# Optimization experiments

Hardware: AMD Instinct MI355X
Metric: run time of the kernel (lower is better)

## Reference

```python
import jax, jax.numpy as jnp
import numpy as np

N = 50000      # nodes
E = 800000     # edges (avg degree 16)
D = 128        # hidden dim
L = 3          # message-passing layers
NU = 1         # DRew nu -> delay = max(k - nu, 0)


def setup_inputs() -> dict:
    key = jax.random.key(0)
    ks = jax.random.split(key, 6)
    x = jax.random.normal(ks[0], (N, D), dtype=jnp.float32)
    edge_index = jax.random.randint(ks[1], (2, E), 0, N)          # [2, E] (src, dst)
    edge_attr = jax.random.randint(ks[2], (E,), 1, L + 1)          # edge types in {1..L}
    scale = 1.0 / np.sqrt(D).astype(np.float32)
    Ws = jax.random.normal(ks[3], (L, D, D), dtype=jnp.float32) * scale       # mlp_s per layer
    bs = jnp.zeros((L, D), dtype=jnp.float32)
    Wk = jax.random.normal(ks[4], (L, L, D, D), dtype=jnp.float32) * scale    # mlp_k, padded; layer t uses k=1..t+1
    bk = jnp.zeros((L, L, D), dtype=jnp.float32)
    eps = jnp.zeros((L,), dtype=jnp.float32)
    return dict(x=x, edge_index=edge_index, edge_attr=edge_attr,
                Ws=Ws, bs=bs, Wk=Wk, bk=bk, eps=eps)


def reference(x, edge_index, edge_attr, Ws, bs, Wk, bk, eps):
    src, dst = edge_index[0], edge_index[1]
    xs = [x]
    for t in range(L):
        xt = xs[-1]
        # out = (1 + eps) * mlp_s(x)
        out = (1.0 + eps[t]) * jax.nn.relu(xt @ Ws[t] + bs[t])
        for k in range(1, t + 2):
            delay = max(k - NU, 0)
            x_src = xs[t - delay]                       # delayed node features
            mask = (edge_attr == k).astype(xt.dtype)    # edge-type mask (replaces boolean column select)
            msg = x_src[src] * mask[:, None]            # gather + mask: [E, D]
            agg = jax.ops.segment_sum(msg, dst, num_segments=N)  # scatter-add per destination
            out = out + jax.nn.relu(agg @ Wk[t, k - 1] + bk[t, k - 1])  # mlp_k(k)
        # gin_nn_post is an empty Sequential -> identity; then F.relu; then residual
        h = jax.nn.relu(out)
        xs.append(xt + h)
    return xs[-1]
```

## Files before the change

kernel.cpp:

```cpp
#include <hip/hip_runtime.h>
#include <hip/hip_bf16.h>


#define NODES 50000
#define EDGES 800000
#define DIM   128
#define ND    ((long)NODES * DIM)
#define NB3   (3 * NODES)
#define NPART 8
#define PSIZE (NODES / NPART)
#define NROWP 50048
#define NBLKS ((NB3 + 255) / 256)
#define NCELL 192
#define SORTN (NCELL * NBLKS)

typedef __attribute__((ext_vector_type(8))) short  bf16x8;
typedef __attribute__((ext_vector_type(4))) float  f32x4;

#define LDS_STRIDE 136

__global__ __launch_bounds__(256) void init_kernel(
    const float* __restrict__ x, const float* __restrict__ Ws,
    const float* __restrict__ Wk, __hip_bfloat16* __restrict__ xb0,
    __hip_bfloat16* __restrict__ xb1, __hip_bfloat16* __restrict__ xb2,
    __hip_bfloat16* __restrict__ WT, int* __restrict__ cursor) {
  int b = blockIdx.x, tid = threadIdx.x;
  long i = (long)b * 256 + tid;
  if (i < ND / 4) {
    float4 v = ((const float4*)x)[i];
    union { __hip_bfloat16 h[4]; uint2 u; } pk;
    pk.h[0] = __float2bfloat16(v.x); pk.h[1] = __float2bfloat16(v.y);
    pk.h[2] = __float2bfloat16(v.z); pk.h[3] = __float2bfloat16(v.w);
    ((uint2*)xb0)[i] = pk.u;
  }
  if (b < 12) {
    const float* src = (b < 3) ? (Ws + (long)b * 16384) : (Wk + (long)(b - 3) * 16384);
    __hip_bfloat16* dst = WT + (long)b * 16384;
    for (int idx = tid; idx < 16384; idx += 256) {
      int k = idx >> 7, n = idx & 127;
      dst[n * 128 + k] = __float2bfloat16(src[idx]);
    }
  }
  if (b >= 12 && b < 12 + NBLKS) {
    int g = (b - 12) * 256 + tid;
    if (g < NB3) cursor[g] = 0;
  }
  if (b == 599 && tid < DIM) {
    xb0[(long)NODES * DIM + tid] = __float2bfloat16(0.f);
    xb1[(long)NODES * DIM + tid] = __float2bfloat16(0.f);
    xb2[(long)NODES * DIM + tid] = __float2bfloat16(0.f);
  }
}

__global__ __launch_bounds__(256) void hist_kernel(
    const int* __restrict__ ei, const int* __restrict__ attr,
    int* __restrict__ counts, int E) {
  int e = blockIdx.x * 256 + threadIdx.x;
  if (e >= E) return;
  atomicAdd(&counts[ei[E + e] * 3 + (attr[e] - 1)], 1);
}

__global__ __launch_bounds__(256) void scan_a_kernel(
    const int* __restrict__ counts, int* __restrict__ partial,
    int* __restrict__ blocksums, int n) {
  __shared__ int tmp[256];
  int gid = blockIdx.x * 256 + threadIdx.x;
  int v = (gid < n) ? ((counts[gid] + 3) & ~3) : 0;
  tmp[threadIdx.x] = v;
  __syncthreads();
  for (int off = 1; off < 256; off <<= 1) {
    int t = (threadIdx.x >= off) ? tmp[threadIdx.x - off] : 0;
    __syncthreads();
    tmp[threadIdx.x] += t;
    __syncthreads();
  }
  if (gid < n) partial[gid] = tmp[threadIdx.x] - v;
  if (threadIdx.x == 255) blocksums[blockIdx.x] = tmp[255];
}

__global__ __launch_bounds__(256) void scan_b_kernel(int* __restrict__ bs, int nb) {
  __shared__ int tmp[256];
  __shared__ int carry;
  if (threadIdx.x == 0) carry = 0;
  __syncthreads();
  for (int base = 0; base < nb; base += 256) {
    int gid = base + threadIdx.x;
    int v = (gid < nb) ? bs[gid] : 0;
    tmp[threadIdx.x] = v;
    __syncthreads();
    for (int off = 1; off < 256; off <<= 1) {
      int t = (threadIdx.x >= off) ? tmp[threadIdx.x - off] : 0;
      __syncthreads();
      tmp[threadIdx.x] += t;
      __syncthreads();
    }
    if (gid < nb) bs[gid] = tmp[threadIdx.x] - v + carry;
    __syncthreads();
    if (threadIdx.x == 0) carry += tmp[255];
    __syncthreads();
  }
}

__global__ __launch_bounds__(256) void scanc_bhist_kernel(
    int* __restrict__ rowptr, int* __restrict__ cursor,
    const int* __restrict__ bs, int* __restrict__ csr,
    int* __restrict__ G, int n) {
  __shared__ int h[NCELL];
  if (threadIdx.x < NCELL) h[threadIdx.x] = 0;
  __syncthreads();
  int gid = blockIdx.x * 256 + threadIdx.x;
  if (gid < n) {
    int cnt = cursor[gid];
    int pcnt = (cnt + 3) & ~3;
    int val = rowptr[gid] + bs[blockIdx.x];
    rowptr[gid] = val;
    cursor[gid] = val;
    for (int i = cnt; i < pcnt; ++i) csr[val + i] = NODES;
    if (gid == n - 1) rowptr[n] = val + pcnt;
    int c = pcnt >> 2; if (c > 63) c = 63;
    int km1 = gid - (gid / 3) * 3;
    atomicAdd(&h[km1 * 64 + (63 - c)], 1);
  }
  __syncthreads();
  if (threadIdx.x < NCELL) G[threadIdx.x * NBLKS + blockIdx.x] = h[threadIdx.x];
}

__global__ __launch_bounds__(256) void fill_kernel(
    const int* __restrict__ ei, const int* __restrict__ attr,
    int* __restrict__ cursor, int* __restrict__ csr_src, int E) {
  int p = blockIdx.x & (NPART - 1);
  int chunk = blockIdx.x >> 3;
  int e = chunk * 256 + threadIdx.x;
  if (e >= E) return;
  int d = ei[E + e];
  int lo = p * PSIZE;
  if (d < lo || d >= lo + PSIZE) return;
  int pos = atomicAdd(&cursor[d * 3 + (attr[e] - 1)], 1);
  csr_src[pos] = ei[e];
}

__global__ __launch_bounds__(256) void fscan_a_kernel(
    const int* __restrict__ in, int* __restrict__ partial,
    int* __restrict__ blocksums, int n) {
  __shared__ int tmp[256];
  int gid = blockIdx.x * 256 + threadIdx.x;
  int v = (gid < n) ? in[gid] : 0;
  tmp[threadIdx.x] = v;
  __syncthreads();
  for (int off = 1; off < 256; off <<= 1) {
    int t = (threadIdx.x >= off) ? tmp[threadIdx.x - off] : 0;
    __syncthreads();
    tmp[threadIdx.x] += t;
    __syncthreads();
  }
  if (gid < n) partial[gid] = tmp[threadIdx.x] - v;
  if (threadIdx.x == 255) blocksums[blockIdx.x] = tmp[255];
}

__global__ __launch_bounds__(256) void bfill_kernel(
    const int* __restrict__ rowptr, const int* __restrict__ G,
    const int* __restrict__ bsum2, int* __restrict__ wl) {
  __shared__ int base[NCELL];
  if (threadIdx.x < NCELL) {
    int gidx = threadIdx.x * NBLKS + blockIdx.x;
    base[threadIdx.x] = G[gidx] + bsum2[gidx >> 8];
  }
  __syncthreads();
  int b = blockIdx.x * 256 + threadIdx.x;
  if (b >= NB3) return;
  int pcnt = rowptr[b + 1] - rowptr[b];
  int c = pcnt >> 2; if (c > 63) c = 63;
  int km1 = b - (b / 3) * 3;
  int pos = atomicAdd(&base[km1 * 64 + (63 - c)], 1);
  wl[pos] = b;
}

__global__ __launch_bounds__(256, 6) void gather_kernel(
    const __hip_bfloat16* __restrict__ s0,
    const __hip_bfloat16* __restrict__ s1,
    const __hip_bfloat16* __restrict__ s2,
    const int* __restrict__ rowptr, const int* __restrict__ csr,
    const int* __restrict__ wl,
    __hip_bfloat16* __restrict__ ag0, __hip_bfloat16* __restrict__ ag1,
    __hip_bfloat16* __restrict__ ag2, int nwork) {
  int group = (blockIdx.x * 256 + threadIdx.x) >> 4;
  int lane16 = threadIdx.x & 15;
  if (group >= nwork) return;
  int b = wl[group];
  int d = b / 3;
  int km1 = b - d * 3;
  const __hip_bfloat16* xb = (km1 == 0) ? s0 : ((km1 == 1) ? s1 : s2);
  __hip_bfloat16* ag = (km1 == 0) ? ag0 : ((km1 == 1) ? ag1 : ag2);
  int beg = rowptr[b], end = rowptr[b + 1];
  float a0 = 0.f, a1 = 0.f, a2 = 0.f, a3 = 0.f,
        a4 = 0.f, a5 = 0.f, a6 = 0.f, a7 = 0.f;
  for (int base = beg; base < end; base += 16) {
    int idxv = csr[base + lane16];
    int cnt = end - base; if (cnt > 16) cnt = 16;
    for (int j = 0; j < cnt; j += 4) {
      int q0 = __shfl(idxv, j + 0, 16);
      int q1 = __shfl(idxv, j + 1, 16);
      int q2 = __shfl(idxv, j + 2, 16);
      int q3 = __shfl(idxv, j + 3, 16);
      uint4 v0 = *(const uint4*)(xb + (long)q0 * DIM + lane16 * 8);
      uint4 v1 = *(const uint4*)(xb + (long)q1 * DIM + lane16 * 8);
      uint4 v2 = *(const uint4*)(xb + (long)q2 * DIM + lane16 * 8);
      uint4 v3 = *(const uint4*)(xb + (long)q3 * DIM + lane16 * 8);
      a0 += __uint_as_float(v0.x << 16) + __uint_as_float(v1.x << 16)
          + __uint_as_float(v2.x << 16) + __uint_as_float(v3.x << 16);
      a1 += __uint_as_float(v0.x & 0xffff0000u) + __uint_as_float(v1.x & 0xffff0000u)
          + __uint_as_float(v2.x & 0xffff0000u) + __uint_as_float(v3.x & 0xffff0000u);
      a2 += __uint_as_float(v0.y << 16) + __uint_as_float(v1.y << 16)
          + __uint_as_float(v2.y << 16) + __uint_as_float(v3.y << 16);
      a3 += __uint_as_float(v0.y & 0xffff0000u) + __uint_as_float(v1.y & 0xffff0000u)
          + __uint_as_float(v2.y & 0xffff0000u) + __uint_as_float(v3.y & 0xffff0000u);
      a4 += __uint_as_float(v0.z << 16) + __uint_as_float(v1.z << 16)
          + __uint_as_float(v2.z << 16) + __uint_as_float(v3.z << 16);
      a5 += __uint_as_float(v0.z & 0xffff0000u) + __uint_as_float(v1.z & 0xffff0000u)
          + __uint_as_float(v2.z & 0xffff0000u) + __uint_as_float(v3.z & 0xffff0000u);
      a6 += __uint_as_float(v0.w << 16) + __uint_as_float(v1.w << 16)
          + __uint_as_float(v2.w << 16) + __uint_as_float(v3.w << 16);
      a7 += __uint_as_float(v0.w & 0xffff0000u) + __uint_as_float(v1.w & 0xffff0000u)
          + __uint_as_float(v2.w & 0xffff0000u) + __uint_as_float(v3.w & 0xffff0000u);
    }
  }
  union { __hip_bfloat16 h[8]; uint4 u; } pk;
  pk.h[0] = __float2bfloat16(a0); pk.h[1] = __float2bfloat16(a1);
  pk.h[2] = __float2bfloat16(a2); pk.h[3] = __float2bfloat16(a3);
  pk.h[4] = __float2bfloat16(a4); pk.h[5] = __float2bfloat16(a5);
  pk.h[6] = __float2bfloat16(a6); pk.h[7] = __float2bfloat16(a7);
  *(uint4*)(ag + (long)d * DIM + lane16 * 8) = pk.u;
}

__global__ __launch_bounds__(256, 4) void lgemm_kernel(
    const __hip_bfloat16* __restrict__ xbSelf,
    const __hip_bfloat16* __restrict__ ag0,
    const __hip_bfloat16* __restrict__ ag1,
    const __hip_bfloat16* __restrict__ ag2,
    const __hip_bfloat16* __restrict__ WT,
    const float* __restrict__ bs_t,
    const float* __restrict__ bk_t,
    const float* __restrict__ epsp,
    __hip_bfloat16* __restrict__ xnb,
    float* __restrict__ xn,
    int t) {
  __shared__ __hip_bfloat16 b_lds[128 * LDS_STRIDE];

  int tid = threadIdx.x;
  long row0 = (long)blockIdx.x * 64;
  int wave = tid >> 6, lane = tid & 63;
  int l15 = lane & 15, q = lane >> 4;
  long arow = row0 + wave * 16 + l15;

  const __hip_bfloat16* Asrc[4] = {xbSelf, ag0, ag1, ag2};
  f32x4 out[8];

  for (int p = 0; p <= t + 1; ++p) {
    if (p > 0) __syncthreads();
    const __hip_bfloat16* Am = Asrc[p];
    uint4 af[4];
#pragma unroll
    for (int k0i = 0; k0i < 4; ++k0i)
      af[k0i] = *(const uint4*)(Am + arow * DIM + k0i * 32 + 8 * q);
    const __hip_bfloat16* W = (p == 0) ? (WT + (long)t * 16384)
                                       : (WT + (long)(3 + t * 3 + (p - 1)) * 16384);
    {
      const uint4* bq = (const uint4*)W;
#pragma unroll
      for (int i = 0; i < 8; ++i) {
        int idx = tid + 256 * i;
        int n = idx >> 4, k8 = idx & 15;
        uint4 v = bq[idx];
        *(uint4*)(b_lds + n * LDS_STRIDE + k8 * 8) = v;
      }
    }
    __syncthreads();

    f32x4 acc[8] = {};
#pragma unroll
    for (int k0i = 0; k0i < 4; ++k0i) {
      bf16x8 a = __builtin_bit_cast(bf16x8, af[k0i]);
#pragma unroll
      for (int j = 0; j < 8; ++j) {
        bf16x8 bfr = *(const bf16x8*)(b_lds + (16 * j + l15) * LDS_STRIDE + k0i * 32 + 8 * q);
        acc[j] = __builtin_amdgcn_mfma_f32_16x16x32_bf16(a, bfr, acc[j], 0, 0, 0);
      }
    }
    if (p == 0) {
      float sc = 1.0f + *epsp;
#pragma unroll
      for (int j = 0; j < 8; ++j) {
        float b = bs_t[16 * j + l15];
#pragma unroll
        for (int r = 0; r < 4; ++r) out[j][r] = sc * fmaxf(acc[j][r] + b, 0.f);
      }
    } else {
      const float* bb = bk_t + (p - 1) * 128;
#pragma unroll
      for (int j = 0; j < 8; ++j) {
        float b = bb[16 * j + l15];
#pragma unroll
        for (int r = 0; r < 4; ++r) out[j][r] += fmaxf(acc[j][r] + b, 0.f);
      }
    }
  }

  long rbase = row0 + wave * 16 + q * 4;
  bool fin = (xn != nullptr);
#pragma unroll
  for (int j = 0; j < 8; ++j) {
    int col = 16 * j + l15;
#pragma unroll
    for (int r = 0; r < 4; ++r) {
      long grow = rbase + r;
      if (grow < NODES) {
        float res = __bfloat162float(xbSelf[grow * DIM + col]);
        float v = res + fmaxf(out[j][r], 0.f);
        if (fin) xn[grow * DIM + col] = v;
        else     xnb[grow * DIM + col] = __float2bfloat16(v);
      }
    }
  }
}

extern "C" void kernel_launch(void* const* d_in, const int* in_sizes, int n_in,
                              void* d_out, int out_size, void* d_ws, size_t ws_size,
                              hipStream_t stream) {
  const float* x    = (const float*)d_in[0];
  const int*   ei   = (const int*)d_in[1];
  const int*   attr = (const int*)d_in[2];
  const float* Ws   = (const float*)d_in[3];
  const float* bs   = (const float*)d_in[4];
  const float* Wk   = (const float*)d_in[5];
  const float* bk   = (const float*)d_in[6];
  const float* eps  = (const float*)d_in[7];
  float* out = (float*)d_out;

  char* ws = (char*)d_ws;
  size_t off = 0;
  auto alloc = [&](size_t bytes) { char* p = ws + off; off += (bytes + 255) & ~(size_t)255; return p; };
  const size_t ROWB = (size_t)NROWP * DIM * 2;
  __hip_bfloat16* xb0 = (__hip_bfloat16*)alloc(ROWB);
  __hip_bfloat16* xb1 = (__hip_bfloat16*)alloc(ROWB);
  __hip_bfloat16* xb2 = (__hip_bfloat16*)alloc(ROWB);
  __hip_bfloat16* ag0 = (__hip_bfloat16*)alloc(ROWB);
  __hip_bfloat16* ag1 = (__hip_bfloat16*)alloc(ROWB);
  __hip_bfloat16* ag2 = (__hip_bfloat16*)alloc(ROWB);
  __hip_bfloat16* WT  = (__hip_bfloat16*)alloc(12 * 16384 * 2);
  int* cursor    = (int*)alloc((size_t)NB3 * 4);
  int* rowptr    = (int*)alloc((size_t)(NB3 + 1) * 4);
  int* blocksums = (int*)alloc(1024 * 4);
  int* G         = (int*)alloc((size_t)SORTN * 4);
  int* bsum2     = (int*)alloc(1024 * 4);
  int* wl        = (int*)alloc((size_t)NB3 * 4);
  int* csr_src   = (int*)alloc((size_t)(EDGES + 4 * NB3 + 16) * 4);

  int egrid  = (EDGES + 255) / 256;
  int igrid  = (int)(ND / 4 / 256);
  int fgrid  = (SORTN + 255) / 256;

  hipLaunchKernelGGL(init_kernel, dim3(igrid), dim3(256), 0, stream,
                     x, Ws, Wk, xb0, xb1, xb2, WT, cursor);
  hipLaunchKernelGGL(hist_kernel, dim3(egrid), dim3(256), 0, stream, ei, attr, cursor, EDGES);
  hipLaunchKernelGGL(scan_a_kernel, dim3(NBLKS), dim3(256), 0, stream, cursor, rowptr, blocksums, NB3);
  hipLaunchKernelGGL(scan_b_kernel, dim3(1), dim3(256), 0, stream, blocksums, NBLKS);
  hipLaunchKernelGGL(scanc_bhist_kernel, dim3(NBLKS), dim3(256), 0, stream,
                     rowptr, cursor, blocksums, csr_src, G, NB3);
  hipLaunchKernelGGL(fill_kernel, dim3(egrid * NPART), dim3(256), 0, stream, ei, attr, cursor, csr_src, EDGES);
  hipLaunchKernelGGL(fscan_a_kernel, dim3(fgrid), dim3(256), 0, stream, G, G, bsum2, SORTN);
  hipLaunchKernelGGL(scan_b_kernel, dim3(1), dim3(256), 0, stream, bsum2, fgrid);
  hipLaunchKernelGGL(bfill_kernel, dim3(NBLKS), dim3(256), 0, stream, rowptr, G, bsum2, wl);

  int ggrid = (NODES + 63) / 64;
  auto glaunch = [&](int nwork, const __hip_bfloat16* s0, const __hip_bfloat16* s1,
                     const __hip_bfloat16* s2) {
    int blocks = (nwork * 16 + 255) / 256;
    hipLaunchKernelGGL(gather_kernel, dim3(blocks), dim3(256), 0, stream,
                       s0, s1, s2, rowptr, csr_src, wl, ag0, ag1, ag2, nwork);
  };

  glaunch(NODES, xb0, nullptr, nullptr);
  hipLaunchKernelGGL(lgemm_kernel, dim3(ggrid), dim3(256), 0, stream,
                     xb0, ag0, ag1, ag2, WT, bs + 0, bk + 0, eps + 0,
                     xb1, (float*)nullptr, 0);
  glaunch(2 * NODES, xb1, xb0, nullptr);
  hipLaunchKernelGGL(lgemm_kernel, dim3(ggrid), dim3(256), 0, stream,
                     xb1, ag0, ag1, ag2, WT, bs + 128, bk + 3 * 128, eps + 1,
                     xb2, (float*)nullptr, 1);
  glaunch(3 * NODES, xb2, xb1, xb0);
  hipLaunchKernelGGL(lgemm_kernel, dim3(ggrid), dim3(256), 0, stream,
                     xb2, ag0, ag1, ag2, WT, bs + 256, bk + 6 * 128, eps + 2,
                     (__hip_bfloat16*)nullptr, out, 2);
}
```

Measured before the change: 336.6 us.

## Gather each layer's features once for all future edge types; shrink bucket/partition counts

```diff
diff --git a/kernel.cpp b/kernel.cpp
--- a/kernel.cpp
+++ b/kernel.cpp
@@ -7,11 +7,11 @@
 #define DIM   128
 #define ND    ((long)NODES * DIM)
 #define NB3   (3 * NODES)
-#define NPART 8
+#define NPART 4
 #define PSIZE (NODES / NPART)
 #define NROWP 50048
 #define NBLKS ((NB3 + 255) / 256)
-#define NCELL 192
+#define NCELL 96
 #define SORTN (NCELL * NBLKS)
 
 typedef __attribute__((ext_vector_type(8))) short  bf16x8;
@@ -117,9 +117,9 @@
     cursor[gid] = val;
     for (int i = cnt; i < pcnt; ++i) csr[val + i] = NODES;
     if (gid == n - 1) rowptr[n] = val + pcnt;
-    int c = pcnt >> 2; if (c > 63) c = 63;
+    int c = pcnt >> 2; if (c > 31) c = 31;
     int km1 = gid - (gid / 3) * 3;
-    atomicAdd(&h[km1 * 64 + (63 - c)], 1);
+    atomicAdd(&h[km1 * 32 + (31 - c)], 1);
   }
   __syncthreads();
   if (threadIdx.x < NCELL) G[threadIdx.x * NBLKS + blockIdx.x] = h[threadIdx.x];
@@ -129,7 +129,7 @@
     const int* __restrict__ ei, const int* __restrict__ attr,
     int* __restrict__ cursor, int* __restrict__ csr_src, int E) {
   int p = blockIdx.x & (NPART - 1);
-  int chunk = blockIdx.x >> 3;
+  int chunk = blockIdx.x >> 2;
   int e = chunk * 256 + threadIdx.x;
   if (e >= E) return;
   int d = ei[E + e];
@@ -169,16 +169,14 @@
   int b = blockIdx.x * 256 + threadIdx.x;
   if (b >= NB3) return;
   int pcnt = rowptr[b + 1] - rowptr[b];
-  int c = pcnt >> 2; if (c > 63) c = 63;
+  int c = pcnt >> 2; if (c > 31) c = 31;
   int km1 = b - (b / 3) * 3;
-  int pos = atomicAdd(&base[km1 * 64 + (63 - c)], 1);
+  int pos = atomicAdd(&base[km1 * 32 + (31 - c)], 1);
   wl[pos] = b;
 }
 
 __global__ __launch_bounds__(256, 6) void gather_kernel(
-    const __hip_bfloat16* __restrict__ s0,
-    const __hip_bfloat16* __restrict__ s1,
-    const __hip_bfloat16* __restrict__ s2,
+    const __hip_bfloat16* __restrict__ src,
     const int* __restrict__ rowptr, const int* __restrict__ csr,
     const int* __restrict__ wl,
     __hip_bfloat16* __restrict__ ag0, __hip_bfloat16* __restrict__ ag1,
@@ -189,7 +187,6 @@
   int b = wl[group];
   int d = b / 3;
   int km1 = b - d * 3;
-  const __hip_bfloat16* xb = (km1 == 0) ? s0 : ((km1 == 1) ? s1 : s2);
   __hip_bfloat16* ag = (km1 == 0) ? ag0 : ((km1 == 1) ? ag1 : ag2);
   int beg = rowptr[b], end = rowptr[b + 1];
   float a0 = 0.f, a1 = 0.f, a2 = 0.f, a3 = 0.f,
@@ -202,10 +199,10 @@
       int q1 = __shfl(idxv, j + 1, 16);
       int q2 = __shfl(idxv, j + 2, 16);
       int q3 = __shfl(idxv, j + 3, 16);
-      uint4 v0 = *(const uint4*)(xb + (long)q0 * DIM + lane16 * 8);
-      uint4 v1 = *(const uint4*)(xb + (long)q1 * DIM + lane16 * 8);
-      uint4 v2 = *(const uint4*)(xb + (long)q2 * DIM + lane16 * 8);
-      uint4 v3 = *(const uint4*)(xb + (long)q3 * DIM + lane16 * 8);
+      uint4 v0 = *(const uint4*)(src + (long)q0 * DIM + lane16 * 8);
+      uint4 v1 = *(const uint4*)(src + (long)q1 * DIM + lane16 * 8);
+      uint4 v2 = *(const uint4*)(src + (long)q2 * DIM + lane16 * 8);
+      uint4 v3 = *(const uint4*)(src + (long)q3 * DIM + lane16 * 8);
       a0 += __uint_as_float(v0.x << 16) + __uint_as_float(v1.x << 16)
           + __uint_as_float(v2.x << 16) + __uint_as_float(v3.x << 16);
       a1 += __uint_as_float(v0.x & 0xffff0000u) + __uint_as_float(v1.x & 0xffff0000u)
@@ -340,13 +337,16 @@
   size_t off = 0;
   auto alloc = [&](size_t bytes) { char* p = ws + off; off += (bytes + 255) & ~(size_t)255; return p; };
   const size_t ROWB = (size_t)NROWP * DIM * 2;
-  __hip_bfloat16* xb0 = (__hip_bfloat16*)alloc(ROWB);
-  __hip_bfloat16* xb1 = (__hip_bfloat16*)alloc(ROWB);
-  __hip_bfloat16* xb2 = (__hip_bfloat16*)alloc(ROWB);
-  __hip_bfloat16* ag0 = (__hip_bfloat16*)alloc(ROWB);
-  __hip_bfloat16* ag1 = (__hip_bfloat16*)alloc(ROWB);
-  __hip_bfloat16* ag2 = (__hip_bfloat16*)alloc(ROWB);
-  __hip_bfloat16* WT  = (__hip_bfloat16*)alloc(12 * 16384 * 2);
+  __hip_bfloat16* xb0  = (__hip_bfloat16*)alloc(ROWB);
+  __hip_bfloat16* xb1  = (__hip_bfloat16*)alloc(ROWB);
+  __hip_bfloat16* xb2  = (__hip_bfloat16*)alloc(ROWB);
+  __hip_bfloat16* agA0 = (__hip_bfloat16*)alloc(ROWB);
+  __hip_bfloat16* agA1 = (__hip_bfloat16*)alloc(ROWB);
+  __hip_bfloat16* agA2 = (__hip_bfloat16*)alloc(ROWB);
+  __hip_bfloat16* agB0 = (__hip_bfloat16*)alloc(ROWB);
+  __hip_bfloat16* agB1 = (__hip_bfloat16*)alloc(ROWB);
+  __hip_bfloat16* agC0 = (__hip_bfloat16*)alloc(ROWB);
+  __hip_bfloat16* WT   = (__hip_bfloat16*)alloc(12 * 16384 * 2);
   int* cursor    = (int*)alloc((size_t)NB3 * 4);
   int* rowptr    = (int*)alloc((size_t)(NB3 + 1) * 4);
   int* blocksums = (int*)alloc(1024 * 4);
@@ -372,23 +372,23 @@
   hipLaunchKernelGGL(bfill_kernel, dim3(NBLKS), dim3(256), 0, stream, rowptr, G, bsum2, wl);
 
   int ggrid = (NODES + 63) / 64;
-  auto glaunch = [&](int nwork, const __hip_bfloat16* s0, const __hip_bfloat16* s1,
-                     const __hip_bfloat16* s2) {
+  auto glaunch = [&](int nwork, const __hip_bfloat16* src, __hip_bfloat16* a0,
+                     __hip_bfloat16* a1, __hip_bfloat16* a2) {
     int blocks = (nwork * 16 + 255) / 256;
     hipLaunchKernelGGL(gather_kernel, dim3(blocks), dim3(256), 0, stream,
-                       s0, s1, s2, rowptr, csr_src, wl, ag0, ag1, ag2, nwork);
+                       src, rowptr, csr_src, wl, a0, a1, a2, nwork);
   };
 
-  glaunch(NODES, xb0, nullptr, nullptr);
+  glaunch(3 * NODES, xb0, agA0, agA1, agA2);
   hipLaunchKernelGGL(lgemm_kernel, dim3(ggrid), dim3(256), 0, stream,
-                     xb0, ag0, ag1, ag2, WT, bs + 0, bk + 0, eps + 0,
+                     xb0, agA0, agA0, agA0, WT, bs + 0, bk + 0, eps + 0,
                      xb1, (float*)nullptr, 0);
-  glaunch(2 * NODES, xb1, xb0, nullptr);
+  glaunch(2 * NODES, xb1, agB0, agB1, agB1);
   hipLaunchKernelGGL(lgemm_kernel, dim3(ggrid), dim3(256), 0, stream,
-                     xb1, ag0, ag1, ag2, WT, bs + 128, bk + 3 * 128, eps + 1,
+                     xb1, agB0, agA1, agA1, WT, bs + 128, bk + 3 * 128, eps + 1,
                      xb2, (float*)nullptr, 1);
-  glaunch(3 * NODES, xb2, xb1, xb0);
+  glaunch(NODES, xb2, agC0, agC0, agC0);
   hipLaunchKernelGGL(lgemm_kernel, dim3(ggrid), dim3(256), 0, stream,
-                     xb2, ag0, ag1, ag2, WT, bs + 256, bk + 6 * 128, eps + 2,
+                     xb2, agC0, agB1, agA2, WT, bs + 256, bk + 6 * 128, eps + 2,
                      (__hip_bfloat16*)nullptr, out, 2);
 }
```

Result: no change. 330.0 us (-2.0%).
